# Performance work log

Hardware: AMD Instinct MI355X
Metric: run time of the kernel (lower is better)

## Reference

```python
import jax, jax.numpy as jnp
from jax import lax
import numpy as np

B, T, C = 32, 2048, 512
CLAMP_LO, CLAMP_HI = 1e-4, 1.0 - 1e-4


def setup_inputs() -> dict:
    key = jax.random.key(0)
    x = jax.random.normal(key, (B, T, C), dtype=jnp.float32)
    # parameter initialized at logit(0.9), repeated per channel
    logit_alpha = jnp.full((C,), float(np.log(0.9 / 0.1)), dtype=jnp.float32)
    delta = jnp.asarray(1.0, dtype=jnp.float32)
    return {"x": x, "logit_alpha": logit_alpha, "delta": delta}


def reference(x, logit_alpha, delta):
    # x: [B, T, C]; logit_alpha: [C]; delta: scalar
    a = jnp.clip(jax.nn.sigmoid(logit_alpha), CLAMP_LO, CLAMP_HI).astype(x.dtype)  # [C]
    one_minus_a = 1.0 - a  # [C], broadcasts over [B, C]
    d = delta.astype(x.dtype)

    def step(y_prev, x_t):  # y_prev, x_t: [B, C]
        r = x_t - y_prev
        g = jnp.where(jnp.abs(r) <= d, r, d * jnp.sign(r))  # Huber gradient
        y = y_prev + one_minus_a * g
        return y, y

    y0 = x[:, 0, :]  # [B, C]
    xs = jnp.swapaxes(x[:, 1:, :], 0, 1)  # [T-1, B, C]
    _, ys = lax.scan(step, y0, xs)  # ys: [T-1, B, C]
    y = jnp.concatenate([y0[None], ys], axis=0)  # [T, B, C]
    return jnp.swapaxes(y, 0, 1)  # [B, T, C]
```

## Files before the change

kernel.cpp:

```cpp
#include <hip/hip_runtime.h>
#include <math.h>


#define TT   2048
#define CC   512
#define TILE 64
#define NTIL (TT / TILE)

__global__ __launch_bounds__(64, 1)
void huber_ema_kernel(const float* __restrict__ x,
                      const float* __restrict__ logit_alpha,
                      const float* __restrict__ delta,
                      float* __restrict__ y)
{
    const int blk  = blockIdx.x;
    const int b    = blk >> 3;
    const int cc   = blk & 7;
    const int lane = threadIdx.x;

    const int chc = (cc << 6) + lane;
    const float la = logit_alpha[chc];
    float a = 1.0f / (1.0f + expf(-la));
    a = fminf(fmaxf(a, 1e-4f), 1.0f - 1e-4f);
    const float oma = 1.0f - a;
    const float d = delta[0];

    const float* __restrict__ xb = x + (size_t)b * TT * CC + (cc << 6);
    float*       __restrict__ yb = y + (size_t)b * TT * CC + (cc << 6);

    const int tl = lane >> 4;
    const int c4 = (lane & 15) << 2;
    const float* __restrict__ xl = xb + (size_t)tl * CC + c4;

    __shared__ float lds[2][TILE * 64];

    float4 xr[16];
    float  xin[TILE];

    float yv = xb[lane];

    #pragma unroll
    for (int g = 0; g < 16; ++g)
        xr[g] = *(const float4*)(xl + (size_t)(g * 4) * CC);
    #pragma unroll
    for (int g = 0; g < 16; ++g)
        *(float4*)&lds[0][g * 256 + (lane << 2)] = xr[g];
    #pragma unroll
    for (int g = 0; g < 16; ++g)
        xr[g] = *(const float4*)(xl + (size_t)(TILE + g * 4) * CC);

    for (int k = 0; k < NTIL; ++k) {
        float* __restrict__ buf  = lds[k & 1];
        float* __restrict__ bufn = lds[(k + 1) & 1];

        if (k + 1 < NTIL) {
            #pragma unroll
            for (int g = 0; g < 16; ++g)
                *(float4*)&bufn[g * 256 + (lane << 2)] = xr[g];
        }
        if (k + 2 < NTIL) {
            #pragma unroll
            for (int g = 0; g < 16; ++g)
                xr[g] = *(const float4*)(xl + (size_t)((k + 2) * TILE + g * 4) * CC);
        }

        #pragma unroll
        for (int i = 0; i < TILE; ++i)
            xin[i] = buf[i * 64 + lane];

        const size_t tb = (size_t)k * TILE;
        #pragma unroll
        for (int i = 0; i < TILE; ++i) {
            float r = xin[i] - yv;
            yv += oma * fminf(fmaxf(r, -d), d);
            yb[(tb + (size_t)i) * CC + lane] = yv;
        }
    }
}

extern "C" void kernel_launch(void* const* d_in, const int* in_sizes, int n_in,
                              void* d_out, int out_size, void* d_ws, size_t ws_size,
                              hipStream_t stream) {
    const float* x  = (const float*)d_in[0];
    const float* la = (const float*)d_in[1];
    const float* dl = (const float*)d_in[2];
    float* y = (float*)d_out;

    huber_ema_kernel<<<dim3(256), dim3(64), 0, stream>>>(x, la, dl, y);
}
```

Before: 264.1 us.

## Stage scan outputs through LDS and write back as float4 rows

Output values are no longer stored straight to global memory one float per timestep. The scan now writes them into a double-buffered LDS tile, and the tile is then copied out with coalesced float4 stores laid out the same way as the input loads. Scheduling barriers pin the order so that the LDS reads of a tile, the prefetch of the next tile, the serial scan and the write-back stay in separate phases. This cuts the number of narrow global store instructions, at the cost of extra LDS traffic and LDS capacity. It depends on a single wavefront of 64 threads being in lockstep, since there is no explicit sync between the LDS write and the read.

```diff
diff --git a/kernel.cpp b/kernel.cpp
--- a/kernel.cpp
+++ b/kernel.cpp
@@ -18,8 +18,7 @@
     const int cc   = blk & 7;
     const int lane = threadIdx.x;
 
-    const int chc = (cc << 6) + lane;
-    const float la = logit_alpha[chc];
+    const float la = logit_alpha[(cc << 6) + lane];
     float a = 1.0f / (1.0f + expf(-la));
     a = fminf(fmaxf(a, 1e-4f), 1.0f - 1e-4f);
     const float oma = 1.0f - a;
@@ -31,49 +30,64 @@
     const int tl = lane >> 4;
     const int c4 = (lane & 15) << 2;
     const float* __restrict__ xl = xb + (size_t)tl * CC + c4;
+    float*       __restrict__ yl = yb + (size_t)tl * CC + c4;
 
-    __shared__ float lds[2][TILE * 64];
+    __shared__ float xs[2][TILE * 64];
+    __shared__ float ys[2][TILE * 64];
 
     float4 xr[16];
-    float  xin[TILE];
 
     float yv = xb[lane];
 
-    #pragma unroll
-    for (int g = 0; g < 16; ++g)
-        xr[g] = *(const float4*)(xl + (size_t)(g * 4) * CC);
-    #pragma unroll
-    for (int g = 0; g < 16; ++g)
-        *(float4*)&lds[0][g * 256 + (lane << 2)] = xr[g];
+    {
+        float4 t0[16];
+        #pragma unroll
+        for (int g = 0; g < 16; ++g)
+            t0[g] = *(const float4*)(xl + (size_t)(g * 4) * CC);
+        #pragma unroll
+        for (int g = 0; g < 16; ++g)
+            *(float4*)&xs[0][g * 256 + (lane << 2)] = t0[g];
+    }
     #pragma unroll
     for (int g = 0; g < 16; ++g)
         xr[g] = *(const float4*)(xl + (size_t)(TILE + g * 4) * CC);
 
     for (int k = 0; k < NTIL; ++k) {
-        float* __restrict__ buf  = lds[k & 1];
-        float* __restrict__ bufn = lds[(k + 1) & 1];
+        const float* __restrict__ bx  = xs[k & 1];
+        float*       __restrict__ bxn = xs[(k + 1) & 1];
+        float*       __restrict__ by  = ys[k & 1];
+
+        float xin[TILE];
+        #pragma unroll
+        for (int i = 0; i < TILE; ++i)
+            xin[i] = bx[i * 64 + lane];
+        __builtin_amdgcn_sched_barrier(0);
 
         if (k + 1 < NTIL) {
             #pragma unroll
             for (int g = 0; g < 16; ++g)
-                *(float4*)&bufn[g * 256 + (lane << 2)] = xr[g];
+                *(float4*)&bxn[g * 256 + (lane << 2)] = xr[g];
         }
         if (k + 2 < NTIL) {
             #pragma unroll
             for (int g = 0; g < 16; ++g)
                 xr[g] = *(const float4*)(xl + (size_t)((k + 2) * TILE + g * 4) * CC);
         }
+        __builtin_amdgcn_sched_barrier(0);
 
-        #pragma unroll
-        for (int i = 0; i < TILE; ++i)
-            xin[i] = buf[i * 64 + lane];
-
-        const size_t tb = (size_t)k * TILE;
         #pragma unroll
         for (int i = 0; i < TILE; ++i) {
             float r = xin[i] - yv;
             yv += oma * fminf(fmaxf(r, -d), d);
-            yb[(tb + (size_t)i) * CC + lane] = yv;
+            by[i * 64 + lane] = yv;
+        }
+        __builtin_amdgcn_sched_barrier(0);
+
+        const size_t tb = (size_t)k * TILE;
+        #pragma unroll
+        for (int g = 0; g < 16; ++g) {
+            float4 v = *(const float4*)&by[g * 256 + (lane << 2)];
+            *(float4*)(yl + (tb + (size_t)(g * 4)) * CC) = v;
         }
     }
 }
```

Measured after the change: 268.1 us. Within noise of the previous version (+1.5%).
